# Kernel optimization log

Hardware: AMD Instinct MI355X
Metric: run time of the kernel (lower is better)

The kernel has to match this reference:

```python
import jax, jax.numpy as jnp
import numpy as np

B, K, N_ANN, C = 8, 100000, 32, 80
ALPHA, GAMMA = 0.25, 0.5


def setup_inputs() -> dict:
    key = jax.random.key(0)
    k1, k2, k3, k4, k5, k6, k7 = jax.random.split(key, 7)
    classifications = jax.random.uniform(k1, (B, K, C), jnp.float32, 0.01, 0.99)
    regressions = jax.random.normal(k2, (B, K, 4), jnp.float32)
    # anchors: valid boxes (x1,y1,x2,y2) on a ~1024px image
    a_ctr = jax.random.uniform(k3, (1, K, 2), jnp.float32, 32.0, 992.0)
    a_wh = jax.random.uniform(k4, (1, K, 2), jnp.float32, 16.0, 256.0)
    anchors = jnp.concatenate([a_ctr - a_wh / 2, a_ctr + a_wh / 2], axis=-1)
    # GT annotations: (x1,y1,x2,y2,label), all valid (label >= 0)
    g_ctr = jax.random.uniform(k5, (B, N_ANN, 2), jnp.float32, 64.0, 960.0)
    g_wh = jax.random.uniform(k6, (B, N_ANN, 2), jnp.float32, 16.0, 256.0)
    labels = jax.random.randint(k7, (B, N_ANN, 1), 0, C).astype(jnp.float32)
    annotations = jnp.concatenate([g_ctr - g_wh / 2, g_ctr + g_wh / 2, labels], axis=-1)
    return {"classifications": classifications, "regressions": regressions,
            "anchors": anchors, "annotations": annotations}


def _calc_iou(a, b):
    # a: [K,4] anchors, b: [N,4] gt boxes -> IoU [K,N]
    area_b = (b[:, 2] - b[:, 0]) * (b[:, 3] - b[:, 1])
    area_a = (a[:, 2] - a[:, 0]) * (a[:, 3] - a[:, 1])
    iw = jnp.clip(jnp.minimum(a[:, None, 2], b[None, :, 2]) - jnp.maximum(a[:, None, 0], b[None, :, 0]), 0.0)
    ih = jnp.clip(jnp.minimum(a[:, None, 3], b[None, :, 3]) - jnp.maximum(a[:, None, 1], b[None, :, 1]), 0.0)
    inter = iw * ih
    union = jnp.clip(area_a[:, None] + area_b[None, :] - inter, 1e-8)
    return inter / union


def _per_image(classification, regression, annotation, anchor):
    p = jnp.clip(classification, 1e-4, 1.0 - 1e-4)
    valid = annotation[:, 4] >= 0  # label == -1 means padding
    iou = _calc_iou(anchor, annotation[:, :4])                  # [K,N]
    iou = jnp.where(valid[None, :], iou, -1.0)
    iou_max = jnp.max(iou, axis=1)                               # [K]
    iou_argmax = jnp.argmax(iou, axis=1)                         # [K]
    positive = iou_max >= 0.5                                    # [K]
    num_pos = jnp.sum(positive.astype(jnp.float32))

    assigned = annotation[iou_argmax]                            # [K,5]
    onehot = jax.nn.one_hot(assigned[:, 4].astype(jnp.int32), C, dtype=p.dtype)  # [K,C]
    # targets: -1 = ignore, 0 = negative, 1 = matched class
    base = jnp.where(iou_max < 0.4, 0.0, -1.0)[:, None]          # [K,1]
    targets = jnp.where(positive[:, None], onehot, base)         # [K,C]

    is_pos_cls = targets == 1.0
    alpha_factor = jnp.where(is_pos_cls, ALPHA, 1.0 - ALPHA)
    focal_weight = alpha_factor * jnp.where(is_pos_cls, 1.0 - p, p) ** GAMMA
    bce = -(targets * jnp.log(p) + (1.0 - targets) * jnp.log(1.0 - p))
    cls_loss = jnp.where(targets != -1.0, focal_weight * bce, 0.0)
    cls_loss = jnp.sum(cls_loss) / jnp.clip(num_pos, 1.0)

    aw = anchor[:, 2] - anchor[:, 0]
    ah = anchor[:, 3] - anchor[:, 1]
    acx = anchor[:, 0] + 0.5 * aw
    acy = anchor[:, 1] + 0.5 * ah
    gw = jnp.clip(assigned[:, 2] - assigned[:, 0], 1.0)
    gh = jnp.clip(assigned[:, 3] - assigned[:, 1], 1.0)
    gcx = assigned[:, 0] + 0.5 * gw
    gcy = assigned[:, 1] + 0.5 * gh
    t = jnp.stack([(gcx - acx) / aw, (gcy - acy) / ah, jnp.log(gw / aw), jnp.log(gh / ah)], axis=1)
    t = t / jnp.array([0.1, 0.1, 0.2, 0.2], dtype=t.dtype)
    diff = jnp.abs(t - regression)                               # [K,4]
    sl1 = jnp.where(diff <= 1.0 / 9.0, 0.5 * 9.0 * diff * diff, diff - 0.5 / 9.0)
    reg_sum = jnp.sum(jnp.where(positive[:, None], sl1, 0.0))
    reg_loss = jnp.where(num_pos > 0, reg_sum / jnp.clip(num_pos * 4.0, 1.0), 0.0)
    return cls_loss, reg_loss


def reference(classifications, regressions, anchors, annotations):
    anchor = anchors[0]
    cls_losses, reg_losses = jax.vmap(_per_image, in_axes=(0, 0, 0, None))(
        classifications, regressions, annotations, anchor)
    # original returns mean over batch (keepdim); pack both scalars into [2]
    return jnp.stack([jnp.mean(cls_losses), jnp.mean(reg_losses)])
```

## Files before the change

### kernel.cpp

```cpp
#include <hip/hip_runtime.h>
#include <math.h>

#define B_ 8
#define K_ 100000
#define NANN 32
#define C_ 80
#define BLOCK 256
#define CHUNK 256
#define LN2 0.69314718056f

__global__ void zero_ws_kernel(float* ws) {
    int i = threadIdx.x;
    if (i < 3 * B_) ws[i] = 0.0f;
}

__device__ __forceinline__ float fast_log2(float x) {
#if __has_builtin(__builtin_amdgcn_logf)
    return __builtin_amdgcn_logf(x);
#else
    return __log2f(x);
#endif
}
__device__ __forceinline__ float fast_sqrt(float x) {
#if __has_builtin(__builtin_amdgcn_sqrtf)
    return __builtin_amdgcn_sqrtf(x);
#else
    return sqrtf(x);
#endif
}

__launch_bounds__(BLOCK)
__global__ void focal_main(const float* __restrict__ cls,
                           const float* __restrict__ reg,
                           const float* __restrict__ anc,
                           const float* __restrict__ ann,
                           float* __restrict__ ws) {
    const int b     = blockIdx.y;
    const int chunk = blockIdx.x;
    const int tid   = threadIdx.x;

    __shared__ float s_ann[NANN * 5];
    __shared__ float s_m[CHUNK];
    __shared__ float s_red[(BLOCK / 64) * 3];

    if (tid < NANN * 5) s_ann[tid] = ann[b * NANN * 5 + tid];
    __syncthreads();

    const int k0 = chunk * CHUNK;
    const int k  = k0 + tid;

    float reg_acc  = 0.0f;
    float np_acc   = 0.0f;
    float cls_corr = 0.0f;
    float m        = 0.0f;

    if (k < K_) {
        float4 a = *(const float4*)(anc + (size_t)k * 4);
        float aw = a.z - a.x, ah = a.w - a.y;
        float area_a = aw * ah;

        float best = -2.0f;
        int bestj = 0;
        for (int j = 0; j < NANN; ++j) {
            float bx1 = s_ann[j * 5 + 0], by1 = s_ann[j * 5 + 1];
            float bx2 = s_ann[j * 5 + 2], by2 = s_ann[j * 5 + 3];
            float lbl = s_ann[j * 5 + 4];
            float area_b = (bx2 - bx1) * (by2 - by1);
            float iw = fmaxf(fminf(a.z, bx2) - fmaxf(a.x, bx1), 0.0f);
            float ih = fmaxf(fminf(a.w, by2) - fmaxf(a.y, by1), 0.0f);
            float inter = iw * ih;
            float uni = fmaxf(area_a + area_b - inter, 1e-8f);
            float iou = inter / uni;
            if (lbl < 0.0f) iou = -1.0f;
            if (iou > best) { best = iou; bestj = j; }
        }

        if (best >= 0.5f) {
            m = 1.0f;
            np_acc = 1.0f;
            int c = (int)s_ann[bestj * 5 + 4];
            float p  = cls[((size_t)b * K_ + k) * C_ + c];
            float pm = 1.0f - p;
            float pos_term = -0.25f * fast_sqrt(pm) * (fast_log2(p)  * LN2);
            float neg_term = -0.75f * fast_sqrt(p)  * (fast_log2(pm) * LN2);
            cls_corr = pos_term - neg_term;

            float gx1 = s_ann[bestj * 5 + 0], gy1 = s_ann[bestj * 5 + 1];
            float gx2 = s_ann[bestj * 5 + 2], gy2 = s_ann[bestj * 5 + 3];
            float gw = fmaxf(gx2 - gx1, 1.0f);
            float gh = fmaxf(gy2 - gy1, 1.0f);
            float gcx = gx1 + 0.5f * gw, gcy = gy1 + 0.5f * gh;
            float acx = a.x + 0.5f * aw, acy = a.y + 0.5f * ah;
            float4 r = *(const float4*)(reg + ((size_t)b * K_ + k) * 4);
            float t0 = ((gcx - acx) / aw) * 10.0f;
            float t1 = ((gcy - acy) / ah) * 10.0f;
            float t2 = (fast_log2(gw / aw) * LN2) * 5.0f;
            float t3 = (fast_log2(gh / ah) * LN2) * 5.0f;
            float d, s;
            d = fabsf(t0 - r.x); s = (d <= 1.0f/9.0f) ? 4.5f*d*d : d - 0.5f/9.0f; reg_acc += s;
            d = fabsf(t1 - r.y); s = (d <= 1.0f/9.0f) ? 4.5f*d*d : d - 0.5f/9.0f; reg_acc += s;
            d = fabsf(t2 - r.z); s = (d <= 1.0f/9.0f) ? 4.5f*d*d : d - 0.5f/9.0f; reg_acc += s;
            d = fabsf(t3 - r.w); s = (d <= 1.0f/9.0f) ? 4.5f*d*d : d - 0.5f/9.0f; reg_acc += s;
        } else if (best < 0.4f) {
            m = 1.0f;
        }
    }
    s_m[tid] = m;
    __syncthreads();

    const int na  = min(CHUNK, K_ - k0);
    const int nf4 = na * (C_ / 4);
    const float4* __restrict__ cp =
        (const float4*)(cls + ((size_t)b * K_ + (size_t)k0) * C_);

    float a0 = 0.0f, a1 = 0.0f, a2 = 0.0f, a3 = 0.0f;

    if (na == CHUNK) {
        const int NIT = CHUNK * (C_ / 4) / BLOCK;
#pragma unroll 5
        for (int it = 0; it < NIT; ++it) {
            int idx = tid + it * BLOCK;
            int a_l = (idx * 3277) >> 16;
            float mm = s_m[a_l];
            float4 x = cp[idx];
            a0 = fmaf(mm, fast_sqrt(x.x) * fast_log2(1.0f - x.x), a0);
            a1 = fmaf(mm, fast_sqrt(x.y) * fast_log2(1.0f - x.y), a1);
            a2 = fmaf(mm, fast_sqrt(x.z) * fast_log2(1.0f - x.z), a2);
            a3 = fmaf(mm, fast_sqrt(x.w) * fast_log2(1.0f - x.w), a3);
        }
    } else {
        for (int idx = tid; idx < nf4; idx += BLOCK) {
            int a_l = (idx * 3277) >> 16;
            float mm = s_m[a_l];
            float4 x = cp[idx];
            a0 = fmaf(mm, fast_sqrt(x.x) * fast_log2(1.0f - x.x), a0);
            a1 = fmaf(mm, fast_sqrt(x.y) * fast_log2(1.0f - x.y), a1);
            a2 = fmaf(mm, fast_sqrt(x.z) * fast_log2(1.0f - x.z), a2);
            a3 = fmaf(mm, fast_sqrt(x.w) * fast_log2(1.0f - x.w), a3);
        }
    }

    float cls_acc = ((a0 + a1) + (a2 + a3)) * (-0.75f * LN2) + cls_corr;

    float v0 = cls_acc, v1 = reg_acc, v2 = np_acc;
    for (int off = 32; off > 0; off >>= 1) {
        v0 += __shfl_down(v0, off, 64);
        v1 += __shfl_down(v1, off, 64);
        v2 += __shfl_down(v2, off, 64);
    }
    int wave = tid >> 6, lane = tid & 63;
    if (lane == 0) {
        s_red[wave * 3 + 0] = v0;
        s_red[wave * 3 + 1] = v1;
        s_red[wave * 3 + 2] = v2;
    }
    __syncthreads();
    if (tid == 0) {
        float c = 0.0f, rg = 0.0f, np = 0.0f;
        for (int w = 0; w < BLOCK / 64; ++w) {
            c  += s_red[w * 3 + 0];
            rg += s_red[w * 3 + 1];
            np += s_red[w * 3 + 2];
        }
        atomicAdd(&ws[b * 3 + 0], c);
        atomicAdd(&ws[b * 3 + 1], rg);
        atomicAdd(&ws[b * 3 + 2], np);
    }
}

__global__ void finalize_kernel(const float* __restrict__ ws, float* __restrict__ out) {
    if (threadIdx.x == 0) {
        float cs = 0.0f, rs = 0.0f;
        for (int b = 0; b < B_; ++b) {
            float c  = ws[b * 3 + 0];
            float r  = ws[b * 3 + 1];
            float np = ws[b * 3 + 2];
            cs += c / fmaxf(np, 1.0f);
            rs += (np > 0.0f) ? r / fmaxf(np * 4.0f, 1.0f) : 0.0f;
        }
        out[0] = cs / (float)B_;
        out[1] = rs / (float)B_;
    }
}

extern "C" void kernel_launch(void* const* d_in, const int* in_sizes, int n_in,
                              void* d_out, int out_size, void* d_ws, size_t ws_size,
                              hipStream_t stream) {
    const float* cls = (const float*)d_in[0];
    const float* reg = (const float*)d_in[1];
    const float* anc = (const float*)d_in[2];
    const float* ann = (const float*)d_in[3];
    float* out = (float*)d_out;
    float* ws  = (float*)d_ws;

    zero_ws_kernel<<<1, 64, 0, stream>>>(ws);

    dim3 grid((K_ + CHUNK - 1) / CHUNK, B_);
    focal_main<<<grid, BLOCK, 0, stream>>>(cls, reg, anc, ann, ws);

    finalize_kernel<<<1, 64, 0, stream>>>(ws, out);
}
```

Before: 378.2 us.

## Prefetch classification stream with nontemporal loads and fold finalize into last block

Issues the first four float4 nontemporal loads of the block's classification tile before the IoU matching phase, then runs a rolling four-deep register prefetch in the dense loop. The goal is to hide memory latency behind the IoU compute and to keep streaming data from polluting the cache. The finalize kernel is removed and replaced by a last-block-done atomic counter, saving one launch. The costs are more registers, custom barrier macros, and a threadfence/atomic ticket in every block.

```diff
diff --git a/kernel.cpp b/kernel.cpp
--- a/kernel.cpp
+++ b/kernel.cpp
@@ -8,10 +8,12 @@
 #define BLOCK 256
 #define CHUNK 256
 #define LN2 0.69314718056f
+#define NBLK_X ((K_ + CHUNK - 1) / CHUNK)
+#define TOTAL_BLOCKS (NBLK_X * B_)
 
 __global__ void zero_ws_kernel(float* ws) {
     int i = threadIdx.x;
-    if (i < 3 * B_) ws[i] = 0.0f;
+    if (i < 3 * B_ + 1) ws[i] = 0.0f;
 }
 
 __device__ __forceinline__ float fast_log2(float x) {
@@ -29,12 +31,29 @@
 #endif
 }
 
+typedef float f32x4_t __attribute__((ext_vector_type(4)));
+
+__device__ __forceinline__ float4 ntload4(const float4* p) {
+#if __has_builtin(__builtin_nontemporal_load)
+    f32x4_t v = __builtin_nontemporal_load((const f32x4_t*)p);
+    return make_float4(v.x, v.y, v.z, v.w);
+#else
+    return *p;
+#endif
+}
+
+#define BAR() do { \
+    asm volatile("s_waitcnt lgkmcnt(0)" ::: "memory"); \
+    __builtin_amdgcn_s_barrier(); \
+} while (0)
+
 __launch_bounds__(BLOCK)
 __global__ void focal_main(const float* __restrict__ cls,
                            const float* __restrict__ reg,
                            const float* __restrict__ anc,
                            const float* __restrict__ ann,
-                           float* __restrict__ ws) {
+                           float* __restrict__ ws,
+                           float* __restrict__ out) {
     const int b     = blockIdx.y;
     const int chunk = blockIdx.x;
     const int tid   = threadIdx.x;
@@ -43,19 +62,34 @@
     __shared__ float s_m[CHUNK];
     __shared__ float s_red[(BLOCK / 64) * 3];
 
-    if (tid < NANN * 5) s_ann[tid] = ann[b * NANN * 5 + tid];
-    __syncthreads();
-
     const int k0 = chunk * CHUNK;
     const int k  = k0 + tid;
+    const bool kval = (k < K_);
+    const bool full = (k0 + CHUNK <= K_);
+
+    const float4* __restrict__ cp =
+        (const float4*)(cls + ((size_t)b * K_ + (size_t)k0) * C_);
+
+    float4 a = make_float4(0.f, 0.f, 0.f, 0.f);
+    if (kval) a = *(const float4*)(anc + (size_t)k * 4);
+
+    float4 buf[4];
+    if (full) {
+#pragma unroll
+        for (int i = 0; i < 4; ++i)
+            buf[i] = ntload4(cp + tid + i * BLOCK);
+    }
+
+    if (tid < NANN * 5 / 4)
+        ((float4*)s_ann)[tid] = ((const float4*)(ann + (size_t)b * NANN * 5))[tid];
+    BAR();
 
     float reg_acc  = 0.0f;
     float np_acc   = 0.0f;
     float cls_corr = 0.0f;
     float m        = 0.0f;
 
-    if (k < K_) {
-        float4 a = *(const float4*)(anc + (size_t)k * 4);
+    if (kval) {
         float aw = a.z - a.x, ah = a.w - a.y;
         float area_a = aw * ah;
 
@@ -106,33 +140,32 @@
         }
     }
     s_m[tid] = m;
-    __syncthreads();
-
-    const int na  = min(CHUNK, K_ - k0);
-    const int nf4 = na * (C_ / 4);
-    const float4* __restrict__ cp =
-        (const float4*)(cls + ((size_t)b * K_ + (size_t)k0) * C_);
+    BAR();
 
     float a0 = 0.0f, a1 = 0.0f, a2 = 0.0f, a3 = 0.0f;
 
-    if (na == CHUNK) {
+    if (full) {
         const int NIT = CHUNK * (C_ / 4) / BLOCK;
-#pragma unroll 5
+#pragma unroll
         for (int it = 0; it < NIT; ++it) {
+            float4 x = buf[it & 3];
+            if (it + 4 < NIT)
+                buf[it & 3] = ntload4(cp + tid + (it + 4) * BLOCK);
             int idx = tid + it * BLOCK;
             int a_l = (idx * 3277) >> 16;
             float mm = s_m[a_l];
-            float4 x = cp[idx];
             a0 = fmaf(mm, fast_sqrt(x.x) * fast_log2(1.0f - x.x), a0);
             a1 = fmaf(mm, fast_sqrt(x.y) * fast_log2(1.0f - x.y), a1);
             a2 = fmaf(mm, fast_sqrt(x.z) * fast_log2(1.0f - x.z), a2);
             a3 = fmaf(mm, fast_sqrt(x.w) * fast_log2(1.0f - x.w), a3);
         }
     } else {
+        const int na  = K_ - k0;
+        const int nf4 = na * (C_ / 4);
         for (int idx = tid; idx < nf4; idx += BLOCK) {
             int a_l = (idx * 3277) >> 16;
             float mm = s_m[a_l];
-            float4 x = cp[idx];
+            float4 x = ntload4(cp + idx);
             a0 = fmaf(mm, fast_sqrt(x.x) * fast_log2(1.0f - x.x), a0);
             a1 = fmaf(mm, fast_sqrt(x.y) * fast_log2(1.0f - x.y), a1);
             a2 = fmaf(mm, fast_sqrt(x.z) * fast_log2(1.0f - x.z), a2);
@@ -154,7 +187,7 @@
         s_red[wave * 3 + 1] = v1;
         s_red[wave * 3 + 2] = v2;
     }
-    __syncthreads();
+    BAR();
     if (tid == 0) {
         float c = 0.0f, rg = 0.0f, np = 0.0f;
         for (int w = 0; w < BLOCK / 64; ++w) {
@@ -165,21 +198,22 @@
         atomicAdd(&ws[b * 3 + 0], c);
         atomicAdd(&ws[b * 3 + 1], rg);
         atomicAdd(&ws[b * 3 + 2], np);
-    }
-}
-
-__global__ void finalize_kernel(const float* __restrict__ ws, float* __restrict__ out) {
-    if (threadIdx.x == 0) {
-        float cs = 0.0f, rs = 0.0f;
-        for (int b = 0; b < B_; ++b) {
-            float c  = ws[b * 3 + 0];
-            float r  = ws[b * 3 + 1];
-            float np = ws[b * 3 + 2];
-            cs += c / fmaxf(np, 1.0f);
-            rs += (np > 0.0f) ? r / fmaxf(np * 4.0f, 1.0f) : 0.0f;
-        }
-        out[0] = cs / (float)B_;
-        out[1] = rs / (float)B_;
+
+        __threadfence();
+        unsigned prev = atomicAdd((unsigned int*)(ws + 3 * B_), 1u);
+        if (prev == (unsigned)(TOTAL_BLOCKS - 1)) {
+            __threadfence();
+            float cs = 0.0f, rs = 0.0f;
+            for (int bb = 0; bb < B_; ++bb) {
+                float cc  = atomicAdd(&ws[bb * 3 + 0], 0.0f);
+                float rr  = atomicAdd(&ws[bb * 3 + 1], 0.0f);
+                float nn  = atomicAdd(&ws[bb * 3 + 2], 0.0f);
+                cs += cc / fmaxf(nn, 1.0f);
+                rs += (nn > 0.0f) ? rr / fmaxf(nn * 4.0f, 1.0f) : 0.0f;
+            }
+            out[0] = cs / (float)B_;
+            out[1] = rs / (float)B_;
+        }
     }
 }
 
@@ -195,8 +229,6 @@
 
     zero_ws_kernel<<<1, 64, 0, stream>>>(ws);
 
-    dim3 grid((K_ + CHUNK - 1) / CHUNK, B_);
-    focal_main<<<grid, BLOCK, 0, stream>>>(cls, reg, anc, ann, ws);
-
-    finalize_kernel<<<1, 64, 0, stream>>>(ws, out);
-}
+    dim3 grid(NBLK_X, B_);
+    focal_main<<<grid, BLOCK, 0, stream>>>(cls, reg, anc, ann, ws, out);
+}
```

Result: slower. 497.4 us (+31.5%).
